# Performance work log

Measured on AMD Instinct MI355X. Metric: run time of the kernel, lower is better.

The kernel has to match this reference:

```python
import jax, jax.numpy as jnp
import numpy as np

B, N, IN_DIM = 32, 8192, 128
H, C = 4, 32
NEG_SLOPE = 0.2


def _xavier(key, shape, fan_in, fan_out):
    limit = np.sqrt(6.0 / (fan_in + fan_out))
    return jax.random.uniform(key, shape, minval=-limit, maxval=limit, dtype=jnp.float32)


def setup_inputs() -> dict:
    key = jax.random.key(0)
    k_x, k_wl, k_wr, k_att = jax.random.split(key, 4)
    x = jax.random.normal(k_x, (B, N, IN_DIM), dtype=jnp.float32)
    W_l = _xavier(k_wl, (IN_DIM, H * C), IN_DIM, H * C)
    b_l = jnp.zeros((H * C,), dtype=jnp.float32)
    W_r = _xavier(k_wr, (IN_DIM, H * C), IN_DIM, H * C)
    b_r = jnp.zeros((H * C,), dtype=jnp.float32)
    att = _xavier(k_att, (H, C), H, C)
    return {"x": x, "W_l": W_l, "b_l": b_l, "W_r": W_r, "b_r": b_r, "att": att}


def reference(x, W_l, b_l, W_r, b_r, att):
    Bs, Ns, _ = x.shape
    # Dense projections -> [B, N, H, C]
    x_l = (x @ W_l + b_l).reshape(Bs, Ns, H, C)
    x_r = (x @ W_r + b_r).reshape(Bs, Ns, H, C)
    # GATv2 additive score for edges (j -> center 0): LeakyReLU(x_l[0] + x_r[j])
    e = jax.nn.leaky_relu(x_l[:, :1, :, :] + x_r, negative_slope=NEG_SLOPE)  # [B,N,H,C]
    logits = jnp.einsum('bnhc,hc->bnh', e, att)  # [B,N,H]
    alpha = jax.nn.softmax(logits, axis=1)
    # Weighted aggregation into the center node; others keep their self-loop x_r
    m_center = jnp.sum(alpha[..., None] * x_r, axis=1, keepdims=True)  # [B,1,H,C]
    out = x_r.at[:, :1, :, :].set(m_center)
    return out.reshape(Bs, Ns, H * C)
```

## Files before the change

kernel.cpp:

```cpp
#include <hip/hip_runtime.h>

#define BATCH 32
#define NROWS 8192
#define IND   128
#define HC    128
#define NEG   0.2f
#define NBLK  32
#define ROWS  64
#define ITERS (NROWS / (NBLK * ROWS))
#define PART_STRIDE 136

typedef __attribute__((ext_vector_type(8))) short short8;
typedef __attribute__((ext_vector_type(4))) float f32x4;

__device__ __forceinline__ unsigned short f2bf(float f) {
    unsigned u = __float_as_uint(f);
    u += 0x7FFFu + ((u >> 16) & 1u);
    return (unsigned short)(u >> 16);
}
__device__ __forceinline__ unsigned pack2(float a, float b) {
    return (unsigned)f2bf(a) | ((unsigned)f2bf(b) << 16);
}

__global__ void gat_center(const float* __restrict__ x, const float* __restrict__ Wl,
                           const float* __restrict__ bl, float* __restrict__ xl0)
{
    const int b = blockIdx.x, t = threadIdx.x;
    __shared__ float xrow[128];
    xrow[t] = x[(size_t)b * NROWS * IND + t];
    __syncthreads();
    float acc = bl[t];
#pragma unroll 16
    for (int k = 0; k < 128; ++k) acc = fmaf(xrow[k], Wl[k * 128 + t], acc);
    xl0[b * 128 + t] = acc;
}

__global__ __launch_bounds__(256, 4) void gat_main(
    const float* __restrict__ x, const float* __restrict__ Wr,
    const float* __restrict__ br, const float* __restrict__ att,
    const float* __restrict__ xl0, float* __restrict__ out,
    float* __restrict__ part)
{
    const int tid  = threadIdx.x;
    const int lane = tid & 63;
    const int wv   = tid >> 6;
    const int b    = blockIdx.x >> 5;
    const int blk  = blockIdx.x & (NBLK - 1);

    __shared__ float ubuf[64 * 132];
    __shared__ float w_s[64][4];
    __shared__ float wmax_s[4][4];
    __shared__ float wsum_s[4][4];
    __shared__ float Mrun_s[4], Srun_s[4], scale_s[4];
    __shared__ float Prun_s[128];
    __shared__ float ptmp_s[2][128];
    __shared__ float xl0_s[128], att_s[128], br_s[128];

    unsigned short* Asw = (unsigned short*)ubuf;
    float (*xr_s)[132]  = (float(*)[132])ubuf;

    for (int i = tid; i < 128 * 128; i += 256) {
        int n = i & 127, k = i >> 7;
        Asw[n * 128 + (k ^ ((n & 7) << 3))] = f2bf(Wr[k * 128 + n]);
    }
    if (tid < 128) {
        xl0_s[tid]  = xl0[b * 128 + tid];
        att_s[tid]  = att[tid];
        br_s[tid]   = br[tid];
        Prun_s[tid] = 0.f;
    }
    if (tid < 4) { Mrun_s[tid] = -INFINITY; Srun_s[tid] = 0.f; }
    __syncthreads();

    short8 bfr[2][4];
    {
        const int ksel = lane >> 4;
#pragma unroll
        for (int ct = 0; ct < 2; ++ct) {
            const int n  = wv * 32 + ct * 16 + (lane & 15);
            const int sw = (n & 7) << 3;
#pragma unroll
            for (int ks = 0; ks < 4; ++ks) {
                int k0 = ks * 32 + ksel * 8;
                bfr[ct][ks] = *(const short8*)&Asw[n * 128 + (k0 ^ sw)];
            }
        }
    }
    __syncthreads();

    const int lr = tid >> 2, lh = tid & 3;

    for (int it = 0; it < ITERS; ++it) {
        const int n0 = blk * (ITERS * ROWS) + it * ROWS;
        const float* xrow0 = x + ((size_t)b * NROWS + n0) * IND;

#pragma unroll
        for (int ii = 0; ii < 4; ++ii) {
            int ci = tid + ii * 256;
            int r  = ci >> 4;
            int kc = (ci & 15) << 3;
            float4 f0 = *(const float4*)(xrow0 + r * IND + kc);
            float4 f1 = *(const float4*)(xrow0 + r * IND + kc + 4);
            uint4 u;
            u.x = pack2(f0.x, f0.y); u.y = pack2(f0.z, f0.w);
            u.z = pack2(f1.x, f1.y); u.w = pack2(f1.z, f1.w);
            *(uint4*)&Asw[r * 128 + (kc ^ ((r & 7) << 3))] = u;
        }
        __syncthreads();

        f32x4 acc[4][2];
#pragma unroll
        for (int i = 0; i < 4; ++i)
#pragma unroll
            for (int j = 0; j < 2; ++j) acc[i][j] = (f32x4){0.f, 0.f, 0.f, 0.f};
        {
            const int ksel = lane >> 4;
#pragma unroll
            for (int rt = 0; rt < 4; ++rt) {
                const int rA  = rt * 16 + (lane & 15);
                const int swa = (rA & 7) << 3;
                short8 afr[4];
#pragma unroll
                for (int ks = 0; ks < 4; ++ks) {
                    int k0 = ks * 32 + ksel * 8;
                    afr[ks] = *(const short8*)&Asw[rA * 128 + (k0 ^ swa)];
                }
#pragma unroll
                for (int ct = 0; ct < 2; ++ct)
#pragma unroll
                    for (int ks = 0; ks < 4; ++ks)
                        acc[rt][ct] = __builtin_amdgcn_mfma_f32_16x16x32_bf16(
                            afr[ks], bfr[ct][ks], acc[rt][ct], 0, 0, 0);
            }
        }
        __syncthreads();

        {
            const int rq = (lane >> 4) * 4;
            const int cb = lane & 15;
#pragma unroll
            for (int rt = 0; rt < 4; ++rt)
#pragma unroll
                for (int ct = 0; ct < 2; ++ct) {
                    const int col  = wv * 32 + ct * 16 + cb;
                    const float bias = br_s[col];
#pragma unroll
                    for (int rg = 0; rg < 4; ++rg)
                        xr_s[rt * 16 + rq + rg][col] = acc[rt][ct][rg] + bias;
                }
        }
        __syncthreads();

        {
            float* ob = out + ((size_t)b * NROWS + n0) * HC;
#pragma unroll
            for (int j = 0; j < 8; ++j) {
                int idx = tid + j * 256;
                int row = idx >> 5, c4 = (idx & 31) << 2;
                *(float4*)(ob + row * HC + c4) = *(const float4*)&xr_s[row][c4];
            }
        }

        float lg = 0.f;
        {
            const float* xp = &xr_s[lr][lh * 32];
            const float* ap = &att_s[lh * 32];
            const float* qp = &xl0_s[lh * 32];
#pragma unroll
            for (int c4 = 0; c4 < 32; c4 += 4) {
                float4 xv = *(const float4*)(xp + c4);
                float4 av = *(const float4*)(ap + c4);
                float4 qv = *(const float4*)(qp + c4);
                float v0 = qv.x + xv.x; v0 = v0 > 0.f ? v0 : NEG * v0;
                float v1 = qv.y + xv.y; v1 = v1 > 0.f ? v1 : NEG * v1;
                float v2 = qv.z + xv.z; v2 = v2 > 0.f ? v2 : NEG * v2;
                float v3 = qv.w + xv.w; v3 = v3 > 0.f ? v3 : NEG * v3;
                lg = fmaf(v0, av.x, fmaf(v1, av.y, fmaf(v2, av.z, fmaf(v3, av.w, lg))));
            }
        }

        float mx = lg;
#pragma unroll
        for (int mk = 4; mk < 64; mk <<= 1) mx = fmaxf(mx, __shfl_xor(mx, mk));
        if (lane < 4) wmax_s[wv][lane] = mx;
        __syncthreads();

        const float Mblk = fmaxf(fmaxf(wmax_s[0][lh], wmax_s[1][lh]),
                                 fmaxf(wmax_s[2][lh], wmax_s[3][lh]));
        const float Mold = Mrun_s[lh];
        const float Mnew = fmaxf(Mold, Mblk);
        const float w    = __expf(lg - Mnew);
        w_s[lr][lh] = w;
        float swv = w;
#pragma unroll
        for (int mk = 4; mk < 64; mk <<= 1) swv += __shfl_xor(swv, mk);
        if (lane < 4) wsum_s[wv][lane] = swv;
        __syncthreads();

        if (tid < 4) {
            const float sc = __expf(Mold - Mnew);
            scale_s[tid] = sc;
            Srun_s[tid]  = Srun_s[tid] * sc +
                (wsum_s[0][tid] + wsum_s[1][tid] + wsum_s[2][tid] + wsum_s[3][tid]);
            Mrun_s[tid]  = Mnew;
        }
        {
            const int hc = tid & 127, half = tid >> 7;
            const int h2 = hc >> 5;
            float accp = 0.f;
#pragma unroll 8
            for (int i2 = 0; i2 < 32; ++i2) {
                int rr = half * 32 + i2;
                accp = fmaf(w_s[rr][h2], xr_s[rr][hc], accp);
            }
            ptmp_s[half][hc] = accp;
        }
        __syncthreads();
        if (tid < 128)
            Prun_s[tid] = Prun_s[tid] * scale_s[tid >> 5] + ptmp_s[0][tid] + ptmp_s[1][tid];
        __syncthreads();
    }

    float* pb = part + (size_t)(b * NBLK + blk) * PART_STRIDE;
    if (tid < 4)   { pb[tid] = Mrun_s[tid]; pb[4 + tid] = Srun_s[tid]; }
    if (tid < 128) pb[8 + tid] = Prun_s[tid];
}

__global__ void gat_final(const float* __restrict__ part, float* __restrict__ out)
{
    const int b = blockIdx.x, t = threadIdx.x;
    const int h = t >> 5;
    const float* pb = part + (size_t)b * NBLK * PART_STRIDE;
    float Mg = -INFINITY;
    for (int i = 0; i < NBLK; ++i) Mg = fmaxf(Mg, pb[i * PART_STRIDE + h]);
    float Sg = 0.f, Pg = 0.f;
    for (int i = 0; i < NBLK; ++i) {
        const float sc = __expf(pb[i * PART_STRIDE + h] - Mg);
        Sg += pb[i * PART_STRIDE + 4 + h] * sc;
        Pg  = fmaf(pb[i * PART_STRIDE + 8 + t], sc, Pg);
    }
    out[(size_t)b * NROWS * HC + t] = Pg / Sg;
}

extern "C" void kernel_launch(void* const* d_in, const int* in_sizes, int n_in,
                              void* d_out, int out_size, void* d_ws, size_t ws_size,
                              hipStream_t stream)
{
    const float* x   = (const float*)d_in[0];
    const float* Wl  = (const float*)d_in[1];
    const float* bl  = (const float*)d_in[2];
    const float* Wr  = (const float*)d_in[3];
    const float* br  = (const float*)d_in[4];
    const float* att = (const float*)d_in[5];
    float* out = (float*)d_out;

    float* xl0  = (float*)d_ws;
    float* part = xl0 + BATCH * 128;

    gat_center<<<BATCH, 128, 0, stream>>>(x, Wl, bl, xl0);
    gat_main<<<BATCH * NBLK, 256, 0, stream>>>(x, Wr, br, att, xl0, out, part);
    gat_final<<<BATCH, 128, 0, stream>>>(part, out);
}
```

Before: 75.93 us.

## Prefetch next x tile into registers and use LDS-only barriers

Global loads for the next 64-row tile of x are issued into registers right after the current tile is packed into LDS. The first tile's loads are also started before the W_r staging, so HBM latency overlaps the MFMA and softmax work. Every __syncthreads is replaced by an inline-asm barrier that waits only on lgkmcnt, so outstanding global loads and stores are not drained at each barrier. The trailing barrier at the end of each iteration is also removed. This adds register pressure from the prefetch buffers, and correctness now depends on the hand-written barrier semantics.

```diff
diff --git a/kernel.cpp b/kernel.cpp
--- a/kernel.cpp
+++ b/kernel.cpp
@@ -13,6 +13,8 @@
 typedef __attribute__((ext_vector_type(8))) short short8;
 typedef __attribute__((ext_vector_type(4))) float f32x4;
 
+#define BARRIER() asm volatile("s_waitcnt lgkmcnt(0)\n\ts_barrier" ::: "memory")
+
 __device__ __forceinline__ unsigned short f2bf(float f) {
     unsigned u = __float_as_uint(f);
     u += 0x7FFFu + ((u >> 16) & 1u);
@@ -59,6 +61,19 @@
     unsigned short* Asw = (unsigned short*)ubuf;
     float (*xr_s)[132]  = (float(*)[132])ubuf;
 
+    const int pr[4] = { (tid) >> 4, (tid + 256) >> 4, (tid + 512) >> 4, (tid + 768) >> 4 };
+    const int pk    = (tid & 15) << 3;
+
+    float4 pf[4][2];
+    {
+        const float* xr0 = x + ((size_t)b * NROWS + blk * (ITERS * ROWS)) * IND;
+#pragma unroll
+        for (int ii = 0; ii < 4; ++ii) {
+            pf[ii][0] = *(const float4*)(xr0 + pr[ii] * IND + pk);
+            pf[ii][1] = *(const float4*)(xr0 + pr[ii] * IND + pk + 4);
+        }
+    }
+
     for (int i = tid; i < 128 * 128; i += 256) {
         int n = i & 127, k = i >> 7;
         Asw[n * 128 + (k ^ ((n & 7) << 3))] = f2bf(Wr[k * 128 + n]);
@@ -70,7 +85,7 @@
         Prun_s[tid] = 0.f;
     }
     if (tid < 4) { Mrun_s[tid] = -INFINITY; Srun_s[tid] = 0.f; }
-    __syncthreads();
+    BARRIER();
 
     short8 bfr[2][4];
     {
@@ -86,27 +101,29 @@
             }
         }
     }
-    __syncthreads();
+    BARRIER();
 
     const int lr = tid >> 2, lh = tid & 3;
 
     for (int it = 0; it < ITERS; ++it) {
         const int n0 = blk * (ITERS * ROWS) + it * ROWS;
-        const float* xrow0 = x + ((size_t)b * NROWS + n0) * IND;
 
 #pragma unroll
         for (int ii = 0; ii < 4; ++ii) {
-            int ci = tid + ii * 256;
-            int r  = ci >> 4;
-            int kc = (ci & 15) << 3;
-            float4 f0 = *(const float4*)(xrow0 + r * IND + kc);
-            float4 f1 = *(const float4*)(xrow0 + r * IND + kc + 4);
             uint4 u;
-            u.x = pack2(f0.x, f0.y); u.y = pack2(f0.z, f0.w);
-            u.z = pack2(f1.x, f1.y); u.w = pack2(f1.z, f1.w);
-            *(uint4*)&Asw[r * 128 + (kc ^ ((r & 7) << 3))] = u;
-        }
-        __syncthreads();
+            u.x = pack2(pf[ii][0].x, pf[ii][0].y); u.y = pack2(pf[ii][0].z, pf[ii][0].w);
+            u.z = pack2(pf[ii][1].x, pf[ii][1].y); u.w = pack2(pf[ii][1].z, pf[ii][1].w);
+            *(uint4*)&Asw[pr[ii] * 128 + (pk ^ ((pr[ii] & 7) << 3))] = u;
+        }
+        if (it + 1 < ITERS) {
+            const float* xr0 = x + ((size_t)b * NROWS + n0 + ROWS) * IND;
+#pragma unroll
+            for (int ii = 0; ii < 4; ++ii) {
+                pf[ii][0] = *(const float4*)(xr0 + pr[ii] * IND + pk);
+                pf[ii][1] = *(const float4*)(xr0 + pr[ii] * IND + pk + 4);
+            }
+        }
+        BARRIER();
 
         f32x4 acc[4][2];
 #pragma unroll
@@ -133,7 +150,7 @@
                             afr[ks], bfr[ct][ks], acc[rt][ct], 0, 0, 0);
             }
         }
-        __syncthreads();
+        BARRIER();
 
         {
             const int rq = (lane >> 4) * 4;
@@ -149,7 +166,7 @@
                         xr_s[rt * 16 + rq + rg][col] = acc[rt][ct][rg] + bias;
                 }
         }
-        __syncthreads();
+        BARRIER();
 
         {
             float* ob = out + ((size_t)b * NROWS + n0) * HC;
@@ -183,7 +200,7 @@
 #pragma unroll
         for (int mk = 4; mk < 64; mk <<= 1) mx = fmaxf(mx, __shfl_xor(mx, mk));
         if (lane < 4) wmax_s[wv][lane] = mx;
-        __syncthreads();
+        BARRIER();
 
         const float Mblk = fmaxf(fmaxf(wmax_s[0][lh], wmax_s[1][lh]),
                                  fmaxf(wmax_s[2][lh], wmax_s[3][lh]));
@@ -195,7 +212,7 @@
 #pragma unroll
         for (int mk = 4; mk < 64; mk <<= 1) swv += __shfl_xor(swv, mk);
         if (lane < 4) wsum_s[wv][lane] = swv;
-        __syncthreads();
+        BARRIER();
 
         if (tid < 4) {
             const float sc = __expf(Mold - Mnew);
@@ -215,10 +232,9 @@
             }
             ptmp_s[half][hc] = accp;
         }
-        __syncthreads();
+        BARRIER();
         if (tid < 128)
             Prun_s[tid] = Prun_s[tid] * scale_s[tid >> 5] + ptmp_s[0][tid] + ptmp_s[1][tid];
-        __syncthreads();
     }
 
     float* pb = part + (size_t)(b * NBLK + blk) * PART_STRIDE;
```

Result: slower. 137.6 us (+81.3%).

## Restructure main kernel: async LDS prefetch of x, register-resident softmax per wave

Applied to the files above, without the earlier changes.

Loads each 64-row tile of x straight into LDS with asynchronous global_load_lds, swizzled, and issues the prefetch of the next tile while the current tile is being processed. Rows are converted to bf16 when they are read for the MFMA. Each wave now owns one head's 32 columns, so logits, the online softmax max/sum and the weighted accumulation all stay in registers and use shuffles instead of shared-memory reductions and many block barriers. Outputs are written directly from the MFMA accumulators, and W_r fragments are read from global memory without staging in LDS. This relies on the wave-to-head mapping and on inline-asm waitcnt barriers being correct, and the direct output stores are strided rather than float4-coalesced.

```diff
diff --git a/kernel.cpp b/kernel.cpp
--- a/kernel.cpp
+++ b/kernel.cpp
@@ -13,6 +13,9 @@
 typedef __attribute__((ext_vector_type(8))) short short8;
 typedef __attribute__((ext_vector_type(4))) float f32x4;
 
+#define BARRIER()  asm volatile("s_waitcnt lgkmcnt(0)\n\ts_barrier" ::: "memory")
+#define WAIT_VM0() asm volatile("s_waitcnt vmcnt(0)" ::: "memory")
+
 __device__ __forceinline__ unsigned short f2bf(float f) {
     unsigned u = __float_as_uint(f);
     u += 0x7FFFu + ((u >> 16) & 1u);
@@ -47,66 +50,56 @@
     const int b    = blockIdx.x >> 5;
     const int blk  = blockIdx.x & (NBLK - 1);
 
-    __shared__ float ubuf[64 * 132];
-    __shared__ float w_s[64][4];
-    __shared__ float wmax_s[4][4];
-    __shared__ float wsum_s[4][4];
-    __shared__ float Mrun_s[4], Srun_s[4], scale_s[4];
-    __shared__ float Prun_s[128];
-    __shared__ float ptmp_s[2][128];
-    __shared__ float xl0_s[128], att_s[128], br_s[128];
-
-    unsigned short* Asw = (unsigned short*)ubuf;
-    float (*xr_s)[132]  = (float(*)[132])ubuf;
-
-    for (int i = tid; i < 128 * 128; i += 256) {
-        int n = i & 127, k = i >> 7;
-        Asw[n * 128 + (k ^ ((n & 7) << 3))] = f2bf(Wr[k * 128 + n]);
-    }
-    if (tid < 128) {
-        xl0_s[tid]  = xl0[b * 128 + tid];
-        att_s[tid]  = att[tid];
-        br_s[tid]   = br[tid];
-        Prun_s[tid] = 0.f;
-    }
-    if (tid < 4) { Mrun_s[tid] = -INFINITY; Srun_s[tid] = 0.f; }
-    __syncthreads();
+    __shared__ float xt[ROWS * IND];
+
+    int goff[8];
+#pragma unroll
+    for (int i = 0; i < 8; ++i) {
+        int D = i * 256 + tid, r = D >> 5, u = (D & 31) ^ (r & 7);
+        goff[i] = r * IND + u * 4;
+    }
+    const size_t xorg = ((size_t)b * NROWS + blk * (ITERS * ROWS)) * IND;
+
+    {
+        const float* src = x + xorg;
+#pragma unroll
+        for (int i = 0; i < 8; ++i)
+            __builtin_amdgcn_global_load_lds(
+                (const __attribute__((address_space(1))) unsigned*)(src + goff[i]),
+                (__attribute__((address_space(3))) unsigned*)(xt + (i * 256 + tid) * 4),
+                16, 0, 0);
+    }
 
     short8 bfr[2][4];
     {
         const int ksel = lane >> 4;
 #pragma unroll
         for (int ct = 0; ct < 2; ++ct) {
-            const int n  = wv * 32 + ct * 16 + (lane & 15);
-            const int sw = (n & 7) << 3;
+            const int n = wv * 32 + ct * 16 + (lane & 15);
 #pragma unroll
             for (int ks = 0; ks < 4; ++ks) {
-                int k0 = ks * 32 + ksel * 8;
-                bfr[ct][ks] = *(const short8*)&Asw[n * 128 + (k0 ^ sw)];
-            }
-        }
-    }
-    __syncthreads();
-
-    const int lr = tid >> 2, lh = tid & 3;
+                const int k0 = ks * 32 + ksel * 8;
+                const float* wp = Wr + (size_t)k0 * HC + n;
+                float v0 = wp[0 * HC], v1 = wp[1 * HC], v2 = wp[2 * HC], v3 = wp[3 * HC];
+                float v4 = wp[4 * HC], v5 = wp[5 * HC], v6 = wp[6 * HC], v7 = wp[7 * HC];
+                union { short8 s; unsigned u[4]; } t;
+                t.u[0] = pack2(v0, v1); t.u[1] = pack2(v2, v3);
+                t.u[2] = pack2(v4, v5); t.u[3] = pack2(v6, v7);
+                bfr[ct][ks] = t.s;
+            }
+        }
+    }
+
+    const int   c0 = wv * 32 + (lane & 15), c1 = c0 + 16;
+    const float q0 = xl0[b * 128 + c0], q1 = xl0[b * 128 + c1];
+    const float a0 = att[c0],           a1 = att[c1];
+    const float bi0 = br[c0],           bi1 = br[c1];
+
+    float Mrun = -INFINITY, Srun = 0.f, P0 = 0.f, P1 = 0.f;
 
     for (int it = 0; it < ITERS; ++it) {
-        const int n0 = blk * (ITERS * ROWS) + it * ROWS;
-        const float* xrow0 = x + ((size_t)b * NROWS + n0) * IND;
-
-#pragma unroll
-        for (int ii = 0; ii < 4; ++ii) {
-            int ci = tid + ii * 256;
-            int r  = ci >> 4;
-            int kc = (ci & 15) << 3;
-            float4 f0 = *(const float4*)(xrow0 + r * IND + kc);
-            float4 f1 = *(const float4*)(xrow0 + r * IND + kc + 4);
-            uint4 u;
-            u.x = pack2(f0.x, f0.y); u.y = pack2(f0.z, f0.w);
-            u.z = pack2(f1.x, f1.y); u.w = pack2(f1.z, f1.w);
-            *(uint4*)&Asw[r * 128 + (kc ^ ((r & 7) << 3))] = u;
-        }
-        __syncthreads();
+        WAIT_VM0();
+        BARRIER();
 
         f32x4 acc[4][2];
 #pragma unroll
@@ -117,13 +110,18 @@
             const int ksel = lane >> 4;
 #pragma unroll
             for (int rt = 0; rt < 4; ++rt) {
-                const int rA  = rt * 16 + (lane & 15);
-                const int swa = (rA & 7) << 3;
+                const int rA = rt * 16 + (lane & 15);
+                const int sw = rA & 7;
                 short8 afr[4];
 #pragma unroll
                 for (int ks = 0; ks < 4; ++ks) {
-                    int k0 = ks * 32 + ksel * 8;
-                    afr[ks] = *(const short8*)&Asw[rA * 128 + (k0 ^ swa)];
+                    const int u0 = ks * 8 + ksel * 2;
+                    float4 lo = *(const float4*)&xt[(rA * 32 + (u0 ^ sw)) * 4];
+                    float4 hi = *(const float4*)&xt[(rA * 32 + ((u0 + 1) ^ sw)) * 4];
+                    union { short8 s; unsigned u[4]; } t;
+                    t.u[0] = pack2(lo.x, lo.y); t.u[1] = pack2(lo.z, lo.w);
+                    t.u[2] = pack2(hi.x, hi.y); t.u[3] = pack2(hi.z, hi.w);
+                    afr[ks] = t.s;
                 }
 #pragma unroll
                 for (int ct = 0; ct < 2; ++ct)
@@ -133,97 +131,87 @@
                             afr[ks], bfr[ct][ks], acc[rt][ct], 0, 0, 0);
             }
         }
-        __syncthreads();
+        BARRIER();
+
+        if (it + 1 < ITERS) {
+            const float* src = x + xorg + (size_t)(it + 1) * ROWS * IND;
+#pragma unroll
+            for (int i = 0; i < 8; ++i)
+                __builtin_amdgcn_global_load_lds(
+                    (const __attribute__((address_space(1))) unsigned*)(src + goff[i]),
+                    (__attribute__((address_space(3))) unsigned*)(xt + (i * 256 + tid) * 4),
+                    16, 0, 0);
+        }
+
+#pragma unroll
+        for (int rt = 0; rt < 4; ++rt)
+#pragma unroll
+            for (int rg = 0; rg < 4; ++rg) {
+                acc[rt][0][rg] += bi0;
+                acc[rt][1][rg] += bi1;
+            }
 
         {
-            const int rq = (lane >> 4) * 4;
-            const int cb = lane & 15;
+            float* ob = out + ((size_t)b * NROWS + blk * (ITERS * ROWS) + it * ROWS) * HC;
+#pragma unroll
+            for (int rt = 0; rt < 4; ++rt) {
+                float* rp = ob + (size_t)(rt * 16 + (lane >> 4) * 4) * HC;
+#pragma unroll
+                for (int rg = 0; rg < 4; ++rg) {
+                    rp[rg * HC + c0] = acc[rt][0][rg];
+                    rp[rg * HC + c1] = acc[rt][1][rg];
+                }
+            }
+        }
+
+        float s[4][4];
+#pragma unroll
+        for (int rt = 0; rt < 4; ++rt)
+#pragma unroll
+            for (int rg = 0; rg < 4; ++rg) {
+                float v0 = q0 + acc[rt][0][rg]; v0 = v0 > 0.f ? v0 : NEG * v0;
+                float v1 = q1 + acc[rt][1][rg]; v1 = v1 > 0.f ? v1 : NEG * v1;
+                s[rt][rg] = fmaf(v0, a0, v1 * a1);
+            }
+#pragma unroll
+        for (int mk = 1; mk < 16; mk <<= 1)
 #pragma unroll
             for (int rt = 0; rt < 4; ++rt)
 #pragma unroll
-                for (int ct = 0; ct < 2; ++ct) {
-                    const int col  = wv * 32 + ct * 16 + cb;
-                    const float bias = br_s[col];
-#pragma unroll
-                    for (int rg = 0; rg < 4; ++rg)
-                        xr_s[rt * 16 + rq + rg][col] = acc[rt][ct][rg] + bias;
-                }
-        }
-        __syncthreads();
-
-        {
-            float* ob = out + ((size_t)b * NROWS + n0) * HC;
-#pragma unroll
-            for (int j = 0; j < 8; ++j) {
-                int idx = tid + j * 256;
-                int row = idx >> 5, c4 = (idx & 31) << 2;
-                *(float4*)(ob + row * HC + c4) = *(const float4*)&xr_s[row][c4];
-            }
-        }
-
-        float lg = 0.f;
-        {
-            const float* xp = &xr_s[lr][lh * 32];
-            const float* ap = &att_s[lh * 32];
-            const float* qp = &xl0_s[lh * 32];
-#pragma unroll
-            for (int c4 = 0; c4 < 32; c4 += 4) {
-                float4 xv = *(const float4*)(xp + c4);
-                float4 av = *(const float4*)(ap + c4);
-                float4 qv = *(const float4*)(qp + c4);
-                float v0 = qv.x + xv.x; v0 = v0 > 0.f ? v0 : NEG * v0;
-                float v1 = qv.y + xv.y; v1 = v1 > 0.f ? v1 : NEG * v1;
-                float v2 = qv.z + xv.z; v2 = v2 > 0.f ? v2 : NEG * v2;
-                float v3 = qv.w + xv.w; v3 = v3 > 0.f ? v3 : NEG * v3;
-                lg = fmaf(v0, av.x, fmaf(v1, av.y, fmaf(v2, av.z, fmaf(v3, av.w, lg))));
-            }
-        }
-
-        float mx = lg;
-#pragma unroll
-        for (int mk = 4; mk < 64; mk <<= 1) mx = fmaxf(mx, __shfl_xor(mx, mk));
-        if (lane < 4) wmax_s[wv][lane] = mx;
-        __syncthreads();
-
-        const float Mblk = fmaxf(fmaxf(wmax_s[0][lh], wmax_s[1][lh]),
-                                 fmaxf(wmax_s[2][lh], wmax_s[3][lh]));
-        const float Mold = Mrun_s[lh];
-        const float Mnew = fmaxf(Mold, Mblk);
-        const float w    = __expf(lg - Mnew);
-        w_s[lr][lh] = w;
-        float swv = w;
-#pragma unroll
-        for (int mk = 4; mk < 64; mk <<= 1) swv += __shfl_xor(swv, mk);
-        if (lane < 4) wsum_s[wv][lane] = swv;
-        __syncthreads();
-
-        if (tid < 4) {
-            const float sc = __expf(Mold - Mnew);
-            scale_s[tid] = sc;
-            Srun_s[tid]  = Srun_s[tid] * sc +
-                (wsum_s[0][tid] + wsum_s[1][tid] + wsum_s[2][tid] + wsum_s[3][tid]);
-            Mrun_s[tid]  = Mnew;
-        }
-        {
-            const int hc = tid & 127, half = tid >> 7;
-            const int h2 = hc >> 5;
-            float accp = 0.f;
-#pragma unroll 8
-            for (int i2 = 0; i2 < 32; ++i2) {
-                int rr = half * 32 + i2;
-                accp = fmaf(w_s[rr][h2], xr_s[rr][hc], accp);
-            }
-            ptmp_s[half][hc] = accp;
-        }
-        __syncthreads();
-        if (tid < 128)
-            Prun_s[tid] = Prun_s[tid] * scale_s[tid >> 5] + ptmp_s[0][tid] + ptmp_s[1][tid];
-        __syncthreads();
+                for (int rg = 0; rg < 4; ++rg)
+                    s[rt][rg] += __shfl_xor(s[rt][rg], mk);
+
+        float mx = s[0][0];
+#pragma unroll
+        for (int rt = 0; rt < 4; ++rt)
+#pragma unroll
+            for (int rg = 0; rg < 4; ++rg) mx = fmaxf(mx, s[rt][rg]);
+        mx = fmaxf(mx, __shfl_xor(mx, 16));
+        mx = fmaxf(mx, __shfl_xor(mx, 32));
+        const float Mnew = fmaxf(Mrun, mx);
+        const float sc   = __expf(Mrun - Mnew);
+        float sumw = 0.f, p0 = 0.f, p1 = 0.f;
+#pragma unroll
+        for (int rt = 0; rt < 4; ++rt)
+#pragma unroll
+            for (int rg = 0; rg < 4; ++rg) {
+                const float w = __expf(s[rt][rg] - Mnew);
+                sumw += w;
+                p0 = fmaf(w, acc[rt][0][rg], p0);
+                p1 = fmaf(w, acc[rt][1][rg], p1);
+            }
+        sumw += __shfl_xor(sumw, 16); sumw += __shfl_xor(sumw, 32);
+        p0   += __shfl_xor(p0, 16);   p0   += __shfl_xor(p0, 32);
+        p1   += __shfl_xor(p1, 16);   p1   += __shfl_xor(p1, 32);
+        Srun = Srun * sc + sumw;
+        P0   = P0 * sc + p0;
+        P1   = P1 * sc + p1;
+        Mrun = Mnew;
     }
 
     float* pb = part + (size_t)(b * NBLK + blk) * PART_STRIDE;
-    if (tid < 4)   { pb[tid] = Mrun_s[tid]; pb[4 + tid] = Srun_s[tid]; }
-    if (tid < 128) pb[8 + tid] = Prun_s[tid];
+    if (lane == 0) { pb[wv] = Mrun; pb[4 + wv] = Srun; }
+    if (lane < 16) { pb[8 + c0] = P0; pb[8 + c1] = P1; }
 }
 
 __global__ void gat_final(const float* __restrict__ part, float* __restrict__ out)
```

New measurement: 120.6 us. 58.8% more time.
